# Kernel tuning notes

Hardware: AMD Instinct MI355X
Metric: run time of the kernel (lower is better)

Reference implementation:

```python
import jax, jax.numpy as jnp
import numpy as np

EPS = 1e-8
LN_EPS = 1e-6
B, S_IN, F, D, NH, MLP, L, O = 32, 512, 16, 512, 8, 2048, 4, 8
HD = D // NH

def softplus(x):
    return jnp.log1p(jnp.exp(x))

def apply_rope(x):
    # x: [B, S, D]; RoPE over full d_model, as in the original
    S, d = x.shape[1], x.shape[2]
    x1, x2 = x[..., ::2], x[..., 1::2]
    theta = jnp.arange(S)[:, None] / 10000 ** (jnp.arange(0, d, 2) / d)
    c, s = jnp.cos(theta)[None], jnp.sin(theta)[None]
    x1r = x1 * c - x2 * s
    x2r = x1 * s + x2 * c
    return jnp.stack([x1r, x2r], axis=-1).reshape(x.shape)

def layer_norm(x, g, b):
    mu = jnp.mean(x, axis=-1, keepdims=True)
    var = jnp.mean(jnp.square(x - mu), axis=-1, keepdims=True)
    return (x - mu) * jax.lax.rsqrt(var + LN_EPS) * g + b

def setup_inputs() -> dict:
    key = jax.random.key(0)
    ks = jax.random.split(key, 32)
    n = jax.random.normal
    d = {
        "x": n(ks[0], (B, S_IN, F), jnp.float32),
        "W_in": n(ks[1], (F, D)) * (1.0 / np.sqrt(F)),
        "b_in": jnp.zeros((D,)),
        "cls_tokens": n(ks[2], (1, O, D)) * 0.02,
        "Wqkv": n(ks[3], (L, D, 3 * D)) * (1.0 / np.sqrt(D)),
        "bqkv": jnp.zeros((L, 3 * D)),
        "Wo": n(ks[4], (L, D, D)) * (1.0 / np.sqrt(D)),
        "bo": jnp.zeros((L, D)),
        "ln1_g": jnp.ones((L, D)), "ln1_b": jnp.zeros((L, D)),
        "Wm1": n(ks[5], (L, D, MLP)) * (1.0 / np.sqrt(D)),
        "bm1": jnp.zeros((L, MLP)),
        "Wm2": n(ks[6], (L, MLP, D)) * (1.0 / np.sqrt(MLP)),
        "bm2": jnp.zeros((L, D)),
        "ln2_g": jnp.ones((L, D)), "ln2_b": jnp.zeros((L, D)),
        "Wh": n(ks[7], (O, D, D)) * (1.0 / np.sqrt(D)),
        "bh": jnp.zeros((O, D)),
        "mu_wmu": n(ks[8], (O, D)) * (1.0 / np.sqrt(D)),
        "mu_wrho": n(ks[9], (O, D)) * 0.001,
        "mu_bmu": jnp.zeros((O,)),
        "mu_brho": n(ks[10], (O,)) * 0.001,
        "lv_wmu": n(ks[11], (O, D)) * (1.0 / np.sqrt(D)),
        "lv_wrho": n(ks[12], (O, D)) * 0.001,
        "lv_bmu": jnp.zeros((O,)),
        "lv_brho": n(ks[13], (O,)) * 0.001,
        "eps_mu_w": n(ks[14], (O, D)),
        "eps_mu_b": n(ks[15], (O,)),
        "eps_lv_w": n(ks[16], (O, D)),
        "eps_lv_b": n(ks[17], (O,)),
    }
    return d

def reference(x, W_in, b_in, cls_tokens, Wqkv, bqkv, Wo, bo, ln1_g, ln1_b,
              Wm1, bm1, Wm2, bm2, ln2_g, ln2_b, Wh, bh,
              mu_wmu, mu_wrho, mu_bmu, mu_brho,
              lv_wmu, lv_wrho, lv_bmu, lv_brho,
              eps_mu_w, eps_mu_b, eps_lv_w, eps_lv_b):
    h = x @ W_in + b_in                                     # [B, S_IN, D]
    cls = jnp.tile(cls_tokens, (h.shape[0], 1, 1))
    h = jnp.concatenate([cls, h], axis=1)                   # [B, S, D]
    Bt, S, d = h.shape
    for l in range(L):
        qkv = h @ Wqkv[l] + bqkv[l]
        q, k, v = jnp.split(qkv, 3, axis=-1)
        q, k = apply_rope(q), apply_rope(k)
        q = q.reshape(Bt, S, NH, HD).transpose(0, 2, 1, 3)
        k = k.reshape(Bt, S, NH, HD).transpose(0, 2, 1, 3)
        v = v.reshape(Bt, S, NH, HD).transpose(0, 2, 1, 3)
        scores = jnp.einsum('bhid,bhjd->bhij', q, k) / jnp.sqrt(jnp.float32(HD))
        attn = jax.nn.softmax(scores, axis=-1)              # dropout off (eval)
        out = jnp.einsum('bhij,bhjd->bhid', attn, v)
        out = out.transpose(0, 2, 1, 3).reshape(Bt, S, d)
        out = out @ Wo[l] + bo[l]
        h = layer_norm(h + out, ln1_g[l], ln1_b[l])
        m = jax.nn.relu(h @ Wm1[l] + bm1[l]) @ Wm2[l] + bm2[l]
        h = layer_norm(h + m, ln2_g[l], ln2_b[l])
    x_cls = h[:, :O, :]                                     # [B, O, D]
    hid = jax.nn.relu(jnp.einsum('bod,odh->boh', x_cls, Wh) + bh[None])
    def var_head(wmu, wrho, bmu, brho, ew, eb):
        w = wmu + (softplus(wrho) + EPS) * ew               # [O, D]
        b = bmu + (softplus(brho) + EPS) * eb               # [O]
        return jnp.einsum('boh,oh->bo', hid, w) + b[None]
    mu = var_head(mu_wmu, mu_wrho, mu_bmu, mu_brho, eps_mu_w, eps_mu_b)
    lv = var_head(lv_wmu, lv_wrho, lv_bmu, lv_brho, eps_lv_w, eps_lv_b)
    lv = jnp.log(EPS + softplus(lv))
    return (mu, lv)
```

## Files before the change

### kernel.cpp

```cpp
#include <hip/hip_runtime.h>
#include <cstdint>


#define BATCH   32
#define SEQ     520
#define SP      576
#define DIM     512
#define NHEAD   8
#define HDIM    64
#define MLPD    2048
#define NLAYER  4
#define NROW    (BATCH * SEQ)
#define NPAIR   256

typedef __attribute__((ext_vector_type(4))) float  f32x4;
typedef __attribute__((ext_vector_type(8))) short  short8;

__device__ __forceinline__ unsigned short f2bf(float f) {
    unsigned u = __float_as_uint(f);
    unsigned r = (u + 0x7fffu + ((u >> 16) & 1u)) >> 16;
    return (unsigned short)r;
}
__device__ __forceinline__ float bf2f(short s) {
    return __uint_as_float(((unsigned)(unsigned short)s) << 16);
}
__device__ __forceinline__ unsigned cvt_pk_bf16(float lo, float hi) {
    unsigned r;
    asm("v_cvt_pk_bf16_f32 %0, %1, %2" : "=v"(r) : "v"(lo), "v"(hi));
    return r;
}
__device__ __forceinline__ float exp2_hw(float x) {
    float r;
    asm("v_exp_f32 %0, %1" : "=v"(r) : "v"(x));
    return r;
}
__device__ __forceinline__ float wred_sum(float v) {
    #pragma unroll
    for (int off = 32; off; off >>= 1) v += __shfl_xor(v, off);
    return v;
}

__device__ __forceinline__ void gload16(const void* g, void* l) {
    __builtin_amdgcn_global_load_lds(
        (const __attribute__((address_space(1))) unsigned int*)g,
        (__attribute__((address_space(3))) unsigned int*)l,
        16, 0, 0);
}

__global__ __launch_bounds__(256) void k_wconv(const float* __restrict__ src,
                                               short* __restrict__ dst,
                                               int K, int N) {
    src += (size_t)blockIdx.z * K * N;
    dst += (size_t)blockIdx.z * K * N;
    int n0 = blockIdx.x * 64, k0 = blockIdx.y * 64;
    __shared__ float t[64][65];
    int tid = threadIdx.x;
    int r = tid >> 2, cq = (tid & 3) * 16;
    const float* sp = src + (size_t)(k0 + r) * N + n0 + cq;
    #pragma unroll
    for (int e = 0; e < 16; e += 4) {
        float4 v = *(const float4*)(sp + e);
        t[r][cq + e] = v.x; t[r][cq + e + 1] = v.y;
        t[r][cq + e + 2] = v.z; t[r][cq + e + 3] = v.w;
    }
    __syncthreads();
    int n = tid >> 2, kq = (tid & 3) * 16;
    short* dp = dst + (size_t)(n0 + n) * K + k0 + kq;
    unsigned o0[4], o1[4];
    #pragma unroll
    for (int e = 0; e < 4; e++)
        o0[e] = cvt_pk_bf16(t[kq + 2 * e][n], t[kq + 2 * e + 1][n]);
    #pragma unroll
    for (int e = 0; e < 4; e++)
        o1[e] = cvt_pk_bf16(t[kq + 8 + 2 * e][n], t[kq + 9 + 2 * e][n]);
    *(uint4*)dp = make_uint4(o0[0], o0[1], o0[2], o0[3]);
    *(uint4*)(dp + 8) = make_uint4(o1[0], o1[1], o1[2], o1[3]);
}

__global__ void k_rope_tab(float2* __restrict__ tab) {
    int s = blockIdx.x, i = threadIdx.x;
    float fr = powf(10000.f, -2.f * (float)i / 512.f);
    float th = (float)s * fr;
    float sn, cn;
    sincosf(th, &sn, &cn);
    tab[s * NPAIR + i] = make_float2(cn, sn);
}

__global__ __launch_bounds__(256) void k_in_proj(const float* __restrict__ x,
                                                 const float* __restrict__ Wi,
                                                 const float* __restrict__ bi,
                                                 const float* __restrict__ cls,
                                                 short* __restrict__ hb) {
    int row = blockIdx.x;
    int b = row / SEQ, s = row % SEQ;
    bool is_cls = s < 8;
    float xr[16];
    if (!is_cls) {
        const float* xp = x + (size_t)(b * 512 + (s - 8)) * 16;
        #pragma unroll
        for (int f = 0; f < 16; f++) xr[f] = xp[f];
    }
    for (int c = threadIdx.x; c < DIM; c += 256) {
        float v;
        if (is_cls) {
            v = cls[s * DIM + c];
        } else {
            v = bi[c];
            #pragma unroll
            for (int f = 0; f < 16; f++) v = fmaf(xr[f], Wi[f * DIM + c], v);
        }
        hb[(size_t)row * DIM + c] = (short)f2bf(v);
    }
}

template <int BK, bool RELU, bool ADDRES>
__global__ __launch_bounds__(512) void k_gemm(const short* __restrict__ A,
                                              const short* __restrict__ Bt,
                                              const float* __restrict__ bias,
                                              const short* __restrict__ Res,
                                              short* __restrict__ Cout,
                                              int N, int K) {
    constexpr int NB  = BK / 8;
    constexpr int MSK = NB - 1;
    constexpr int SH  = (BK == 32) ? 1 : 0;
    constexpr int RPW = 64 / NB;
    constexpr int GPM = 128 / (8 * RPW);
    constexpr int NLD = 2 * GPM;
    __shared__ __align__(16) short As[2][128 * BK];
    __shared__ __align__(16) short Bs[2][128 * BK];
    const int tid = threadIdx.x;
    const int w = tid >> 6, l = tid & 63;

    const int chunk = gridDim.x >> 3;
    const int t = (blockIdx.x & 7) * chunk + (blockIdx.x >> 3);
    const int C = N >> 7;
    const int brow = (t / C) * 128, bcol = (t % C) * 128;

    const int srow = l / NB;
    const int sblk = l & MSK;
    const int soff = ((sblk ^ ((srow >> SH) & MSK)) * 8);
    const int fr = l & 15, t4 = l >> 4;
    const int wr = (w >> 2) * 64;
    const int wc = (w & 3) * 32;

    const short* Ab = A  + (size_t)(brow + w * RPW + srow) * K + soff;
    const short* Bb = Bt + (size_t)(bcol + w * RPW + srow) * K + soff;

    f32x4 acc[4][2];
    #pragma unroll
    for (int m = 0; m < 4; m++)
        #pragma unroll
        for (int n = 0; n < 2; n++) acc[m][n] = (f32x4){0.f, 0.f, 0.f, 0.f};

    auto stage = [&](int ko, int pb) {
        #pragma unroll
        for (int i = 0; i < GPM; i++)
            gload16(Ab + (size_t)(i * 8 * RPW) * K + ko,
                    &As[pb][(i * 8 * RPW + w * RPW) * BK]);
        #pragma unroll
        for (int i = 0; i < GPM; i++)
            gload16(Bb + (size_t)(i * 8 * RPW) * K + ko,
                    &Bs[pb][(i * 8 * RPW + w * RPW) * BK]);
    };

    const int nk = K / BK;
    stage(0, 0);
    stage(BK, 1);

    for (int kt = 0; kt < nk; ++kt) {
        const int cur = kt & 1;
        if (kt + 1 < nk) {
            if constexpr (NLD == 4) asm volatile("s_waitcnt vmcnt(4)" ::: "memory");
            else                    asm volatile("s_waitcnt vmcnt(2)" ::: "memory");
        } else {
            asm volatile("s_waitcnt vmcnt(0)" ::: "memory");
        }
        __builtin_amdgcn_s_barrier();
        __builtin_amdgcn_sched_barrier(0);

        short8 af[4][BK / 32], bf[2][BK / 32];
        #pragma unroll
        for (int m = 0; m < 4; m++) {
            int r = wr + m * 16 + fr;
            #pragma unroll
            for (int kk = 0; kk < BK / 32; kk++)
                af[m][kk] = *(const short8*)
                    &As[cur][r * BK + (((kk * 4 + t4) ^ ((r >> SH) & MSK)) * 8)];
        }
        #pragma unroll
        for (int n = 0; n < 2; n++) {
            int r = wc + n * 16 + fr;
            #pragma unroll
            for (int kk = 0; kk < BK / 32; kk++)
                bf[n][kk] = *(const short8*)
                    &Bs[cur][r * BK + (((kk * 4 + t4) ^ ((r >> SH) & MSK)) * 8)];
        }
        asm volatile("s_waitcnt lgkmcnt(0)" ::: "memory");
        __builtin_amdgcn_s_barrier();
        __builtin_amdgcn_sched_barrier(0);
        if (kt + 2 < nk) stage((kt + 2) * BK, cur);

        __builtin_amdgcn_s_setprio(1);
        #pragma unroll
        for (int kk = 0; kk < BK / 32; kk++)
            #pragma unroll
            for (int m = 0; m < 4; m++)
                #pragma unroll
                for (int n = 0; n < 2; n++)
                    acc[m][n] = __builtin_amdgcn_mfma_f32_16x16x32_bf16(
                        af[m][kk], bf[n][kk], acc[m][n], 0, 0, 0);
        __builtin_amdgcn_s_setprio(0);
    }

    const int r0 = (l >> 4) * 4, c0 = l & 15;
    #pragma unroll
    for (int m = 0; m < 4; m++) {
        #pragma unroll
        for (int n = 0; n < 2; n++) {
            int col = bcol + wc + n * 16 + c0;
            float bv = bias[col];
            #pragma unroll
            for (int q = 0; q < 4; q++) {
                int row = brow + wr + m * 16 + r0 + q;
                float v = acc[m][n][q] + bv;
                if (ADDRES) v += bf2f(Res[(size_t)row * N + col]);
                if (RELU) v = fmaxf(v, 0.f);
                Cout[(size_t)row * N + col] = (short)f2bf(v);
            }
        }
    }
}

template <int BK, bool RELU, bool ADDRES>
__global__ __launch_bounds__(256) void k_gemm64(const short* __restrict__ A,
                                                const short* __restrict__ Bt,
                                                const float* __restrict__ bias,
                                                const short* __restrict__ Res,
                                                short* __restrict__ Cout,
                                                int N, int K) {
    constexpr int NB  = BK / 8;
    constexpr int MSK = NB - 1;
    constexpr int SH  = (BK == 32) ? 1 : 0;
    constexpr int RPL = 512 / BK;
    constexpr int ALW = 128 / (4 * RPL);
    constexpr int BLW = 64 / (4 * RPL);
    constexpr int NLD = ALW + BLW;
    __shared__ __align__(16) short As[2][128 * BK];
    __shared__ __align__(16) short Bs[2][64 * BK];
    const int tid = threadIdx.x;
    const int w = tid >> 6, l = tid & 63;

    const int chunk = gridDim.x >> 3;
    const int t = (blockIdx.x & 7) * chunk + (blockIdx.x >> 3);
    const int C = N >> 6;
    const int brow = (t / C) * 128, bcol = (t % C) * 64;

    const int srow = l / NB;
    const int sblk = l & MSK;
    const int soff = ((sblk ^ ((srow >> SH) & MSK)) * 8);
    const int fr = l & 15, t4 = l >> 4;
    const int wr = (w >> 1) * 64;
    const int wc = (w & 1) * 32;

    f32x4 acc[4][2];
    #pragma unroll
    for (int m = 0; m < 4; m++)
        #pragma unroll
        for (int n = 0; n < 2; n++) acc[m][n] = (f32x4){0.f, 0.f, 0.f, 0.f};

    auto stage = [&](int ko, int pb) {
        #pragma unroll
        for (int i = 0; i < ALW; i++)
            gload16(A + (size_t)(brow + (w * ALW + i) * RPL + srow) * K + ko + soff,
                    &As[pb][((w * ALW + i) * RPL) * BK]);
        #pragma unroll
        for (int i = 0; i < BLW; i++)
            gload16(Bt + (size_t)(bcol + (w * BLW + i) * RPL + srow) * K + ko + soff,
                    &Bs[pb][((w * BLW + i) * RPL) * BK]);
    };

    const int nk = K / BK;
    stage(0, 0);
    stage(BK, 1);

    for (int kt = 0; kt < nk; ++kt) {
        const int cur = kt & 1;
        if (kt + 1 < nk) {
            if constexpr (NLD == 3) asm volatile("s_waitcnt vmcnt(3)" ::: "memory");
            else                    asm volatile("s_waitcnt vmcnt(6)" ::: "memory");
        } else {
            asm volatile("s_waitcnt vmcnt(0)" ::: "memory");
        }
        __builtin_amdgcn_s_barrier();
        __builtin_amdgcn_sched_barrier(0);

        short8 af[4][BK / 32], bf[2][BK / 32];
        #pragma unroll
        for (int m = 0; m < 4; m++) {
            int r = wr + m * 16 + fr;
            #pragma unroll
            for (int kk = 0; kk < BK / 32; kk++)
                af[m][kk] = *(const short8*)
                    &As[cur][r * BK + (((kk * 4 + t4) ^ ((r >> SH) & MSK)) * 8)];
        }
        #pragma unroll
        for (int n = 0; n < 2; n++) {
            int r = wc + n * 16 + fr;
            #pragma unroll
            for (int kk = 0; kk < BK / 32; kk++)
                bf[n][kk] = *(const short8*)
                    &Bs[cur][r * BK + (((kk * 4 + t4) ^ ((r >> SH) & MSK)) * 8)];
        }
        asm volatile("s_waitcnt lgkmcnt(0)" ::: "memory");
        __builtin_amdgcn_s_barrier();
        __builtin_amdgcn_sched_barrier(0);
        if (kt + 2 < nk) stage((kt + 2) * BK, cur);

        __builtin_amdgcn_s_setprio(1);
        #pragma unroll
        for (int kk = 0; kk < BK / 32; kk++)
            #pragma unroll
            for (int m = 0; m < 4; m++)
                #pragma unroll
                for (int n = 0; n < 2; n++)
                    acc[m][n] = __builtin_amdgcn_mfma_f32_16x16x32_bf16(
                        af[m][kk], bf[n][kk], acc[m][n], 0, 0, 0);
        __builtin_amdgcn_s_setprio(0);
    }

    const int r0 = (l >> 4) * 4, c0 = l & 15;
    #pragma unroll
    for (int m = 0; m < 4; m++) {
        #pragma unroll
        for (int n = 0; n < 2; n++) {
            int col = bcol + wc + n * 16 + c0;
            float bv = bias[col];
            #pragma unroll
            for (int q = 0; q < 4; q++) {
                int row = brow + wr + m * 16 + r0 + q;
                float v = acc[m][n][q] + bv;
                if (ADDRES) v += bf2f(Res[(size_t)row * N + col]);
                if (RELU) v = fmaxf(v, 0.f);
                Cout[(size_t)row * N + col] = (short)f2bf(v);
            }
        }
    }
}

__global__ __launch_bounds__(256) void k_kvprep(const short* __restrict__ qkv,
                                                const float2* __restrict__ tab,
                                                short* __restrict__ kbuf,
                                                short* __restrict__ vtbuf) {
    int bx = blockIdx.x;
    int jt = bx % 9, bh = bx / 9, b = bh >> 3, h = bh & 7;
    int tid = threadIdx.x;
    int row = tid >> 2, ch = tid & 3;
    int s = jt * 64 + row;
    bool valid = s < SEQ;
    size_t g = (size_t)(b * SEQ + (valid ? s : 0)) * 1536;

    short8 ok0 = (short8)0, ok1 = (short8)0;
    if (valid) {
        short8 k0 = *(const short8*)(qkv + g + 512 + h * 64 + ch * 16);
        short8 k1 = *(const short8*)(qkv + g + 512 + h * 64 + ch * 16 + 8);
        unsigned* u0 = (unsigned*)&ok0;
        unsigned* u1 = (unsigned*)&ok1;
        #pragma unroll
        for (int pp = 0; pp < 4; pp++) {
            float2 cs = tab[s * NPAIR + h * 32 + ch * 8 + pp];
            float x1 = bf2f(k0[2 * pp]), x2 = bf2f(k0[2 * pp + 1]);
            u0[pp] = cvt_pk_bf16(x1 * cs.x - x2 * cs.y, x1 * cs.y + x2 * cs.x);
            cs = tab[s * NPAIR + h * 32 + ch * 8 + 4 + pp];
            x1 = bf2f(k1[2 * pp]); x2 = bf2f(k1[2 * pp + 1]);
            u1[pp] = cvt_pk_bf16(x1 * cs.x - x2 * cs.y, x1 * cs.y + x2 * cs.x);
        }
    }
    short* kd = kbuf + ((size_t)bh * SP + jt * 64 + row) * 64 + ch * 16;
    *(short8*)kd = ok0;
    *(short8*)(kd + 8) = ok1;

    __shared__ short vt[64][72];
    short8 v0 = (short8)0, v1 = (short8)0;
    if (valid) {
        v0 = *(const short8*)(qkv + g + 1024 + h * 64 + ch * 16);
        v1 = *(const short8*)(qkv + g + 1024 + h * 64 + ch * 16 + 8);
    }
    *(short8*)&vt[row][ch * 16] = v0;
    *(short8*)&vt[row][ch * 16 + 8] = v1;
    __syncthreads();
    int d = row;
    short8 w0, w1;
    #pragma unroll
    for (int e = 0; e < 8; e++) w0[e] = vt[ch * 16 + e][d];
    #pragma unroll
    for (int e = 0; e < 8; e++) w1[e] = vt[ch * 16 + 8 + e][d];
    short* vd = vtbuf + ((size_t)bh * 64 + d) * SP + jt * 64 + ch * 16;
    *(short8*)vd = w0;
    *(short8*)(vd + 8) = w1;
}

__global__ __launch_bounds__(512) void k_attn_mfma(const short* __restrict__ qkv,
                                                   const short* __restrict__ kbuf,
                                                   const short* __restrict__ vtbuf,
                                                   const float2* __restrict__ tab,
                                                   short* __restrict__ aob) {
    __shared__ __align__(16) short Kl[2][64 * 64];
    __shared__ __align__(16) short Vl[2][64 * 64];
    __shared__ __align__(16) short sP[8][16][72];
    const int tid = threadIdx.x;
    const int w = tid >> 6, l = tid & 63;
    const int c = l & 15, t4 = l >> 4;
    int bx = blockIdx.x;
    int qt = bx >> 8, bh = bx & 255, b = bh >> 3, h = bh & 7;

    const float QSC = 0.125f * 1.44269504f;
    int q0 = qt * 128 + w * 16;
    int qrow = q0 + c;
    int qr = qrow < SEQ ? qrow : SEQ - 1;
    size_t gq = (size_t)(b * SEQ + qr) * 1536 + h * 64;
    short8 qf0 = *(const short8*)(qkv + gq + t4 * 8);
    short8 qf1 = *(const short8*)(qkv + gq + 32 + t4 * 8);
    {
        const float2* tq = tab + (size_t)qr * NPAIR + h * 32;
        unsigned* u0 = (unsigned*)&qf0;
        unsigned* u1 = (unsigned*)&qf1;
        #pragma unroll
        for (int pp = 0; pp < 4; pp++) {
            float2 cs = tq[t4 * 4 + pp];
            float x1 = bf2f(qf0[2 * pp]), x2 = bf2f(qf0[2 * pp + 1]);
            u0[pp] = cvt_pk_bf16((x1 * cs.x - x2 * cs.y) * QSC,
                                 (x1 * cs.y + x2 * cs.x) * QSC);
            cs = tq[16 + t4 * 4 + pp];
            x1 = bf2f(qf1[2 * pp]); x2 = bf2f(qf1[2 * pp + 1]);
            u1[pp] = cvt_pk_bf16((x1 * cs.x - x2 * cs.y) * QSC,
                                 (x1 * cs.y + x2 * cs.x) * QSC);
        }
    }

    f32x4 o0 = {0,0,0,0}, o1 = {0,0,0,0}, o2 = {0,0,0,0}, o3 = {0,0,0,0};
    float mrow[4] = {-1e30f, -1e30f, -1e30f, -1e30f};
    float lrow[4] = {0.f, 0.f, 0.f, 0.f};

    const short* kb = kbuf + (size_t)bh * SP * 64;
    const short* vb = vtbuf + (size_t)bh * 64 * SP;
    const int r1 = w * 8 + (l >> 3);
    const int blk = l & 7;

    auto stage = [&](int jt, int pb) {
        gload16(kb + ((size_t)(jt * 64 + r1)) * 64 + ((blk ^ (r1 & 7)) * 8),
                &Kl[pb][(w * 8) * 64]);
        gload16(vb + (size_t)r1 * SP + jt * 64 + ((blk ^ (r1 & 7)) * 8),
                &Vl[pb][(w * 8) * 64]);
    };

    stage(0, 0);
    stage(1, 1);

    for (int jt = 0; jt < 9; jt++) {
        const int cur = jt & 1;
        if (jt + 1 < 9) asm volatile("s_waitcnt vmcnt(2)" ::: "memory");
        else            asm volatile("s_waitcnt vmcnt(0)" ::: "memory");
        __builtin_amdgcn_s_barrier();
        __builtin_amdgcn_sched_barrier(0);

        f32x4 s0 = {0,0,0,0}, s1 = {0,0,0,0}, s2 = {0,0,0,0}, s3 = {0,0,0,0};
        __builtin_amdgcn_s_setprio(1);
        {
            int kr0 = c, kr1 = 16 + c, kr2 = 32 + c, kr3 = 48 + c;
            short8 kf;
            kf = *(const short8*)&Kl[cur][kr0 * 64 + ((t4 ^ (kr0 & 7)) * 8)];
            s0 = __builtin_amdgcn_mfma_f32_16x16x32_bf16(qf0, kf, s0, 0, 0, 0);
            kf = *(const short8*)&Kl[cur][kr0 * 64 + (((4 + t4) ^ (kr0 & 7)) * 8)];
            s0 = __builtin_amdgcn_mfma_f32_16x16x32_bf16(qf1, kf, s0, 0, 0, 0);
            kf = *(const short8*)&Kl[cur][kr1 * 64 + ((t4 ^ (kr1 & 7)) * 8)];
            s1 = __builtin_amdgcn_mfma_f32_16x16x32_bf16(qf0, kf, s1, 0, 0, 0);
            kf = *(const short8*)&Kl[cur][kr1 * 64 + (((4 + t4) ^ (kr1 & 7)) * 8)];
            s1 = __builtin_amdgcn_mfma_f32_16x16x32_bf16(qf1, kf, s1, 0, 0, 0);
            kf = *(const short8*)&Kl[cur][kr2 * 64 + ((t4 ^ (kr2 & 7)) * 8)];
            s2 = __builtin_amdgcn_mfma_f32_16x16x32_bf16(qf0, kf, s2, 0, 0, 0);
            kf = *(const short8*)&Kl[cur][kr2 * 64 + (((4 + t4) ^ (kr2 & 7)) * 8)];
            s2 = __builtin_amdgcn_mfma_f32_16x16x32_bf16(qf1, kf, s2, 0, 0, 0);
            kf = *(const short8*)&Kl[cur][kr3 * 64 + ((t4 ^ (kr3 & 7)) * 8)];
            s3 = __builtin_amdgcn_mfma_f32_16x16x32_bf16(qf0, kf, s3, 0, 0, 0);
            kf = *(const short8*)&Kl[cur][kr3 * 64 + (((4 + t4) ^ (kr3 & 7)) * 8)];
            s3 = __builtin_amdgcn_mfma_f32_16x16x32_bf16(qf1, kf, s3, 0, 0, 0);
        }
        __builtin_amdgcn_s_setprio(0);

        if (jt == 8) {
            #pragma unroll
            for (int r = 0; r < 4; r++) {
                if (c >= 8) s0[r] = -1e30f;
                s1[r] = -1e30f; s2[r] = -1e30f; s3[r] = -1e30f;
            }
        }

        #pragma unroll
        for (int r = 0; r < 4; r++) {
            float pmax = fmaxf(fmaxf(s0[r], s1[r]), fmaxf(s2[r], s3[r]));
            if (!__all(pmax <= mrow[r] + 8.f)) {
                float mx = pmax;
                mx = fmaxf(mx, __shfl_xor(mx, 1));
                mx = fmaxf(mx, __shfl_xor(mx, 2));
                mx = fmaxf(mx, __shfl_xor(mx, 4));
                mx = fmaxf(mx, __shfl_xor(mx, 8));
                if (mx > mrow[r]) {
                    float sc = exp2_hw(mrow[r] - mx);
                    mrow[r] = mx;
                    lrow[r] *= sc;
                    o0[r] *= sc; o1[r] *= sc; o2[r] *= sc; o3[r] *= sc;
                }
            }
            float p0 = exp2_hw(s0[r] - mrow[r]);
            float p1 = exp2_hw(s1[r] - mrow[r]);
            float p2 = exp2_hw(s2[r] - mrow[r]);
            float p3 = exp2_hw(s3[r] - mrow[r]);
            lrow[r] += (p0 + p1) + (p2 + p3);
            unsigned pk01 = cvt_pk_bf16(p0, p1);
            unsigned pk23 = cvt_pk_bf16(p2, p3);
            int q = t4 * 4 + r;
            sP[w][q][c]      = (short)(pk01 & 0xffff);
            sP[w][q][16 + c] = (short)(pk01 >> 16);
            sP[w][q][32 + c] = (short)(pk23 & 0xffff);
            sP[w][q][48 + c] = (short)(pk23 >> 16);
        }

        __builtin_amdgcn_s_setprio(1);
        {
            short8 pf0 = *(const short8*)&sP[w][c][t4 * 8];
            short8 pf1 = *(const short8*)&sP[w][c][32 + t4 * 8];
            int vr0 = c, vr1 = 16 + c, vr2 = 32 + c, vr3 = 48 + c;
            short8 vf;
            vf = *(const short8*)&Vl[cur][vr0 * 64 + ((t4 ^ (vr0 & 7)) * 8)];
            o0 = __builtin_amdgcn_mfma_f32_16x16x32_bf16(pf0, vf, o0, 0, 0, 0);
            vf = *(const short8*)&Vl[cur][vr0 * 64 + (((4 + t4) ^ (vr0 & 7)) * 8)];
            o0 = __builtin_amdgcn_mfma_f32_16x16x32_bf16(pf1, vf, o0, 0, 0, 0);
            vf = *(const short8*)&Vl[cur][vr1 * 64 + ((t4 ^ (vr1 & 7)) * 8)];
            o1 = __builtin_amdgcn_mfma_f32_16x16x32_bf16(pf0, vf, o1, 0, 0, 0);
            vf = *(const short8*)&Vl[cur][vr1 * 64 + (((4 + t4) ^ (vr1 & 7)) * 8)];
            o1 = __builtin_amdgcn_mfma_f32_16x16x32_bf16(pf1, vf, o1, 0, 0, 0);
            vf = *(const short8*)&Vl[cur][vr2 * 64 + ((t4 ^ (vr2 & 7)) * 8)];
            o2 = __builtin_amdgcn_mfma_f32_16x16x32_bf16(pf0, vf, o2, 0, 0, 0);
            vf = *(const short8*)&Vl[cur][vr2 * 64 + (((4 + t4) ^ (vr2 & 7)) * 8)];
            o2 = __builtin_amdgcn_mfma_f32_16x16x32_bf16(pf1, vf, o2, 0, 0, 0);
            vf = *(const short8*)&Vl[cur][vr3 * 64 + ((t4 ^ (vr3 & 7)) * 8)];
            o3 = __builtin_amdgcn_mfma_f32_16x16x32_bf16(pf0, vf, o3, 0, 0, 0);
            vf = *(const short8*)&Vl[cur][vr3 * 64 + (((4 + t4) ^ (vr3 & 7)) * 8)];
            o3 = __builtin_amdgcn_mfma_f32_16x16x32_bf16(pf1, vf, o3, 0, 0, 0);
        }
        __builtin_amdgcn_s_setprio(0);

        asm volatile("s_waitcnt lgkmcnt(0)" ::: "memory");
        __builtin_amdgcn_s_barrier();
        __builtin_amdgcn_sched_barrier(0);
        if (jt + 2 < 9) stage(jt + 2, cur);
    }

    #pragma unroll
    for (int r = 0; r < 4; r++) {
        float s = lrow[r];
        s += __shfl_xor(s, 1);
        s += __shfl_xor(s, 2);
        s += __shfl_xor(s, 4);
        s += __shfl_xor(s, 8);
        int q = q0 + t4 * 4 + r;
        if (q < SEQ) {
            float inv = 1.f / s;
            short* ao = aob + ((size_t)(b * SEQ + q)) * DIM + h * 64 + c;
            ao[0]  = (short)f2bf(o0[r] * inv);
            ao[16] = (short)f2bf(o1[r] * inv);
            ao[32] = (short)f2bf(o2[r] * inv);
            ao[48] = (short)f2bf(o3[r] * inv);
        }
    }
}

__global__ __launch_bounds__(256) void k_ln(short* __restrict__ hb,
                                            const short* __restrict__ sum,
                                            const float* __restrict__ g,
                                            const float* __restrict__ bta) {
    int row = blockIdx.x * 4 + (threadIdx.x >> 6);
    int l = threadIdx.x & 63;
    size_t base = (size_t)row * DIM + l * 8;
    short8 hv = *(const short8*)&sum[base];
    float a[8];
    float s1 = 0.f, s2 = 0.f;
    #pragma unroll
    for (int e = 0; e < 8; e++) {
        a[e] = bf2f(hv[e]);
        s1 += a[e];
        s2 += a[e] * a[e];
    }
    s1 = wred_sum(s1);
    s2 = wred_sum(s2);
    float mu = s1 * (1.f / 512.f);
    float rr = rsqrtf(s2 * (1.f / 512.f) - mu * mu + 1e-6f);
    float4 g0 = *(const float4*)&g[l * 8];
    float4 g1 = *(const float4*)&g[l * 8 + 4];
    float4 b0 = *(const float4*)&bta[l * 8];
    float4 b1 = *(const float4*)&bta[l * 8 + 4];
    unsigned o[4];
    o[0] = cvt_pk_bf16((a[0] - mu) * rr * g0.x + b0.x,
                       (a[1] - mu) * rr * g0.y + b0.y);
    o[1] = cvt_pk_bf16((a[2] - mu) * rr * g0.z + b0.z,
                       (a[3] - mu) * rr * g0.w + b0.w);
    o[2] = cvt_pk_bf16((a[4] - mu) * rr * g1.x + b1.x,
                       (a[5] - mu) * rr * g1.y + b1.y);
    o[3] = cvt_pk_bf16((a[6] - mu) * rr * g1.z + b1.z,
                       (a[7] - mu) * rr * g1.w + b1.w);
    *(uint4*)&hb[base] = make_uint4(o[0], o[1], o[2], o[3]);
}

__global__ __launch_bounds__(256) void k_hid(const short* __restrict__ hb,
                                             const float* __restrict__ Wh,
                                             const float* __restrict__ bh,
                                             float* __restrict__ hid) {
    int j = blockIdx.x * 256 + threadIdx.x;
    int o = blockIdx.y, b = blockIdx.z;
    const short* xr = hb + ((size_t)(b * SEQ + o)) * DIM;
    const float* wcol = Wh + (size_t)o * DIM * DIM + j;
    float acc = bh[o * DIM + j];
    #pragma unroll 8
    for (int d = 0; d < DIM; d++)
        acc = fmaf(bf2f(xr[d]), wcol[(size_t)d * DIM], acc);
    hid[((size_t)b * 8 + o) * DIM + j] = fmaxf(acc, 0.f);
}

__device__ __forceinline__ float softplus_f(float x) { return log1pf(expf(x)); }

__global__ __launch_bounds__(64) void k_var(const float* __restrict__ hid,
                                            const float* __restrict__ mu_wmu,
                                            const float* __restrict__ mu_wrho,
                                            const float* __restrict__ mu_bmu,
                                            const float* __restrict__ mu_brho,
                                            const float* __restrict__ lv_wmu,
                                            const float* __restrict__ lv_wrho,
                                            const float* __restrict__ lv_bmu,
                                            const float* __restrict__ lv_brho,
                                            const float* __restrict__ eps_mu_w,
                                            const float* __restrict__ eps_mu_b,
                                            const float* __restrict__ eps_lv_w,
                                            const float* __restrict__ eps_lv_b,
                                            float* __restrict__ out) {
    const float EPS = 1e-8f;
    int bo = blockIdx.x;
    int o = bo & 7;
    int l = threadIdx.x;
    float am = 0.f, al = 0.f;
    #pragma unroll
    for (int k = 0; k < 8; k++) {
        int d = k * 64 + l;
        int od = o * DIM + d;
        float hv = hid[(size_t)bo * DIM + d];
        am = fmaf(hv, mu_wmu[od] + (softplus_f(mu_wrho[od]) + EPS) * eps_mu_w[od], am);
        al = fmaf(hv, lv_wmu[od] + (softplus_f(lv_wrho[od]) + EPS) * eps_lv_w[od], al);
    }
    am = wred_sum(am);
    al = wred_sum(al);
    if (l == 0) {
        float mu = am + mu_bmu[o] + (softplus_f(mu_brho[o]) + EPS) * eps_mu_b[o];
        out[bo] = mu;
        float lvv = al + lv_bmu[o] + (softplus_f(lv_brho[o]) + EPS) * eps_lv_b[o];
        out[256 + bo] = logf(EPS + softplus_f(lvv));
    }
}

extern "C" void kernel_launch(void* const* d_in, const int* in_sizes, int n_in,
                              void* d_out, int out_size, void* d_ws, size_t ws_size,
                              hipStream_t stream) {
    const float* x      = (const float*)d_in[0];
    const float* W_in   = (const float*)d_in[1];
    const float* b_in   = (const float*)d_in[2];
    const float* cls    = (const float*)d_in[3];
    const float* Wqkv   = (const float*)d_in[4];
    const float* bqkv   = (const float*)d_in[5];
    const float* Wo     = (const float*)d_in[6];
    const float* bo     = (const float*)d_in[7];
    const float* ln1_g  = (const float*)d_in[8];
    const float* ln1_b  = (const float*)d_in[9];
    const float* Wm1    = (const float*)d_in[10];
    const float* bm1    = (const float*)d_in[11];
    const float* Wm2    = (const float*)d_in[12];
    const float* bm2    = (const float*)d_in[13];
    const float* ln2_g  = (const float*)d_in[14];
    const float* ln2_b  = (const float*)d_in[15];
    const float* Wh     = (const float*)d_in[16];
    const float* bh     = (const float*)d_in[17];
    const float* mu_wmu = (const float*)d_in[18];
    const float* mu_wrho= (const float*)d_in[19];
    const float* mu_bmu = (const float*)d_in[20];
    const float* mu_brho= (const float*)d_in[21];
    const float* lv_wmu = (const float*)d_in[22];
    const float* lv_wrho= (const float*)d_in[23];
    const float* lv_bmu = (const float*)d_in[24];
    const float* lv_brho= (const float*)d_in[25];
    const float* e_mu_w = (const float*)d_in[26];
    const float* e_mu_b = (const float*)d_in[27];
    const float* e_lv_w = (const float*)d_in[28];
    const float* e_lv_b = (const float*)d_in[29];
    float* out = (float*)d_out;

    char* p = (char*)d_ws;
    auto alloc = [&](size_t bytes) {
        char* r = p;
        p += (bytes + 255) & ~(size_t)255;
        return r;
    };
    const size_t qkv_bytes = (size_t)NROW * 1536 * 2;
    const size_t kbuf_bytes = (size_t)BATCH * NHEAD * SP * 64 * 2;
    const size_t attn_bytes = qkv_bytes + 2 * kbuf_bytes + 512;
    const size_t mid_bytes = (size_t)NROW * MLPD * 2;
    char*   U1    =          alloc(attn_bytes > mid_bytes ? attn_bytes : mid_bytes);
    short*  qkv   = (short*)U1;
    short*  kbuf  = (short*)(U1 + ((qkv_bytes + 255) & ~(size_t)255));
    short*  vtbuf = kbuf + kbuf_bytes / 2;
    short*  mid   = (short*)U1;
    short*  hb    = (short*) alloc((size_t)NROW * DIM * 2);
    short*  deltab= (short*) alloc((size_t)NROW * DIM * 2);
    short*  aob   = (short*) alloc((size_t)NROW * DIM * 2);
    short*  wqkvt = (short*) alloc((size_t)NLAYER * 1536 * 512 * 2);
    short*  wot   = (short*) alloc((size_t)NLAYER * 512 * 512 * 2);
    short*  wm1t  = (short*) alloc((size_t)NLAYER * 2048 * 512 * 2);
    short*  wm2t  = (short*) alloc((size_t)NLAYER * 512 * 2048 * 2);
    float2* ropet = (float2*)alloc((size_t)SEQ * NPAIR * 8);
    float*  hid   = (float*) alloc((size_t)256 * DIM * 4);

    k_wconv<<<dim3(24, 8, 4), 256, 0, stream>>>(Wqkv, wqkvt, 512, 1536);
    k_wconv<<<dim3(8, 8, 4),  256, 0, stream>>>(Wo,   wot,   512, 512);
    k_wconv<<<dim3(32, 8, 4), 256, 0, stream>>>(Wm1,  wm1t,  512, 2048);
    k_wconv<<<dim3(8, 32, 4), 256, 0, stream>>>(Wm2,  wm2t,  2048, 512);
    k_rope_tab<<<SEQ, NPAIR, 0, stream>>>(ropet);
    k_in_proj<<<NROW, 256, 0, stream>>>(x, W_in, b_in, cls, hb);

    const int RT = NROW / 128;
    for (int l = 0; l < NLAYER; l++) {
        k_gemm<32, false, false><<<RT * 12, 512, 0, stream>>>(
            hb, wqkvt + (size_t)l * 1536 * 512, bqkv + l * 1536, nullptr, qkv, 1536, 512);
        k_kvprep<<<BATCH * NHEAD * 9, 256, 0, stream>>>(qkv, ropet, kbuf, vtbuf);
        k_attn_mfma<<<5 * 256, 512, 0, stream>>>(qkv, kbuf, vtbuf, ropet, aob);
        k_gemm64<32, false, true><<<RT * 8, 256, 0, stream>>>(
            aob, wot + (size_t)l * 512 * 512, bo + l * 512, hb, deltab, 512, 512);
        k_ln<<<NROW / 4, 256, 0, stream>>>(hb, deltab, ln1_g + l * 512, ln1_b + l * 512);
        k_gemm<32, true, false><<<RT * 16, 512, 0, stream>>>(
            hb, wm1t + (size_t)l * 2048 * 512, bm1 + l * 2048, nullptr, mid, 2048, 512);
        k_gemm64<64, false, true><<<RT * 8, 256, 0, stream>>>(
            mid, wm2t + (size_t)l * 512 * 2048, bm2 + l * 512, hb, deltab, 512, 2048);
        k_ln<<<NROW / 4, 256, 0, stream>>>(hb, deltab, ln2_g + l * 512, ln2_b + l * 512);
    }

    k_hid<<<dim3(2, 8, 32), 256, 0, stream>>>(hb, Wh, bh, hid);
    k_var<<<256, 64, 0, stream>>>(hid, mu_wmu, mu_wrho, mu_bmu, mu_brho,
                                  lv_wmu, lv_wrho, lv_bmu, lv_brho,
                                  e_mu_w, e_mu_b, e_lv_w, e_lv_b, out);
}
```

Measured before the change: 1.023 ms.

## Fuse RoPE, Q scaling and K/V layout scatter into QKV GEMM epilogue

The QKV projection GEMM epilogue now applies RoPE to Q and K, using a lane shuffle to fetch each element's pair partner. It pre-scales Q, and writes Q, K and transposed V directly into the per-head buffers that attention consumes. This removes the separate kvprep kernel and the Q RoPE step inside the attention kernel, saving a full read and write of the QKV tensor and one launch per layer. In exchange, the epilogue does scattered 2-byte stores, and the transposed V writes are poorly coalesced. The padded sequence rows of the K/V buffers are no longer zeroed, so they keep leftover data from the aliased MLP buffer.

```diff
diff --git a/kernel.cpp b/kernel.cpp
--- a/kernel.cpp
+++ b/kernel.cpp
@@ -113,12 +113,14 @@
     }
 }
 
-template <int BK, bool RELU, bool ADDRES>
+template <int BK, bool RELU, bool QKVOUT>
 __global__ __launch_bounds__(512) void k_gemm(const short* __restrict__ A,
                                               const short* __restrict__ Bt,
                                               const float* __restrict__ bias,
-                                              const short* __restrict__ Res,
                                               short* __restrict__ Cout,
+                                              short* __restrict__ kb2,
+                                              short* __restrict__ vt2,
+                                              const float2* __restrict__ tab,
                                               int N, int K) {
     constexpr int NB  = BK / 8;
     constexpr int MSK = NB - 1;
@@ -213,6 +215,7 @@
     }
 
     const int r0 = (l >> 4) * 4, c0 = l & 15;
+    const float QSC = 0.125f * 1.44269504f;
     #pragma unroll
     for (int m = 0; m < 4; m++) {
         #pragma unroll
@@ -223,15 +226,36 @@
             for (int q = 0; q < 4; q++) {
                 int row = brow + wr + m * 16 + r0 + q;
                 float v = acc[m][n][q] + bv;
-                if (ADDRES) v += bf2f(Res[(size_t)row * N + col]);
-                if (RELU) v = fmaxf(v, 0.f);
-                Cout[(size_t)row * N + col] = (short)f2bf(v);
+                if (QKVOUT) {
+                    int bb = row / SEQ, s = row - bb * SEQ;
+                    if (col < 1024) {
+                        float vo = __shfl_xor(v, 1);
+                        int i = (col & 511) >> 1;
+                        float2 cs = tab[s * NPAIR + i];
+                        float o = (c0 & 1) ? (vo * cs.y + v * cs.x)
+                                           : (v * cs.x - vo * cs.y);
+                        if (col < 512) {
+                            Cout[(size_t)row * 512 + col] = (short)f2bf(o * QSC);
+                        } else {
+                            int ck = col - 512, h = ck >> 6, d = ck & 63;
+                            kb2[(((size_t)(bb * 8 + h)) * SP + s) * 64 + d] =
+                                (short)f2bf(o);
+                        }
+                    } else {
+                        int cv = col - 1024, h = cv >> 6, d = cv & 63;
+                        vt2[(((size_t)(bb * 8 + h)) * 64 + d) * SP + s] =
+                            (short)f2bf(v);
+                    }
+                } else {
+                    if (RELU) v = fmaxf(v, 0.f);
+                    Cout[(size_t)row * N + col] = (short)f2bf(v);
+                }
             }
         }
     }
 }
 
-template <int BK, bool RELU, bool ADDRES>
+template <int BK, bool ADDRES>
 __global__ __launch_bounds__(256) void k_gemm64(const short* __restrict__ A,
                                                 const short* __restrict__ Bt,
                                                 const float* __restrict__ bias,
@@ -340,69 +364,15 @@
                 int row = brow + wr + m * 16 + r0 + q;
                 float v = acc[m][n][q] + bv;
                 if (ADDRES) v += bf2f(Res[(size_t)row * N + col]);
-                if (RELU) v = fmaxf(v, 0.f);
                 Cout[(size_t)row * N + col] = (short)f2bf(v);
             }
         }
     }
 }
 
-__global__ __launch_bounds__(256) void k_kvprep(const short* __restrict__ qkv,
-                                                const float2* __restrict__ tab,
-                                                short* __restrict__ kbuf,
-                                                short* __restrict__ vtbuf) {
-    int bx = blockIdx.x;
-    int jt = bx % 9, bh = bx / 9, b = bh >> 3, h = bh & 7;
-    int tid = threadIdx.x;
-    int row = tid >> 2, ch = tid & 3;
-    int s = jt * 64 + row;
-    bool valid = s < SEQ;
-    size_t g = (size_t)(b * SEQ + (valid ? s : 0)) * 1536;
-
-    short8 ok0 = (short8)0, ok1 = (short8)0;
-    if (valid) {
-        short8 k0 = *(const short8*)(qkv + g + 512 + h * 64 + ch * 16);
-        short8 k1 = *(const short8*)(qkv + g + 512 + h * 64 + ch * 16 + 8);
-        unsigned* u0 = (unsigned*)&ok0;
-        unsigned* u1 = (unsigned*)&ok1;
-        #pragma unroll
-        for (int pp = 0; pp < 4; pp++) {
-            float2 cs = tab[s * NPAIR + h * 32 + ch * 8 + pp];
-            float x1 = bf2f(k0[2 * pp]), x2 = bf2f(k0[2 * pp + 1]);
-            u0[pp] = cvt_pk_bf16(x1 * cs.x - x2 * cs.y, x1 * cs.y + x2 * cs.x);
-            cs = tab[s * NPAIR + h * 32 + ch * 8 + 4 + pp];
-            x1 = bf2f(k1[2 * pp]); x2 = bf2f(k1[2 * pp + 1]);
-            u1[pp] = cvt_pk_bf16(x1 * cs.x - x2 * cs.y, x1 * cs.y + x2 * cs.x);
-        }
-    }
-    short* kd = kbuf + ((size_t)bh * SP + jt * 64 + row) * 64 + ch * 16;
-    *(short8*)kd = ok0;
-    *(short8*)(kd + 8) = ok1;
-
-    __shared__ short vt[64][72];
-    short8 v0 = (short8)0, v1 = (short8)0;
-    if (valid) {
-        v0 = *(const short8*)(qkv + g + 1024 + h * 64 + ch * 16);
-        v1 = *(const short8*)(qkv + g + 1024 + h * 64 + ch * 16 + 8);
-    }
-    *(short8*)&vt[row][ch * 16] = v0;
-    *(short8*)&vt[row][ch * 16 + 8] = v1;
-    __syncthreads();
-    int d = row;
-    short8 w0, w1;
-    #pragma unroll
-    for (int e = 0; e < 8; e++) w0[e] = vt[ch * 16 + e][d];
-    #pragma unroll
-    for (int e = 0; e < 8; e++) w1[e] = vt[ch * 16 + 8 + e][d];
-    short* vd = vtbuf + ((size_t)bh * 64 + d) * SP + jt * 64 + ch * 16;
-    *(short8*)vd = w0;
-    *(short8*)(vd + 8) = w1;
-}
-
-__global__ __launch_bounds__(512) void k_attn_mfma(const short* __restrict__ qkv,
+__global__ __launch_bounds__(512) void k_attn_mfma(const short* __restrict__ qbuf,
                                                    const short* __restrict__ kbuf,
                                                    const short* __restrict__ vtbuf,
-                                                   const float2* __restrict__ tab,
                                                    short* __restrict__ aob) {
     __shared__ __align__(16) short Kl[2][64 * 64];
     __shared__ __align__(16) short Vl[2][64 * 64];
@@ -413,29 +383,12 @@
     int bx = blockIdx.x;
     int qt = bx >> 8, bh = bx & 255, b = bh >> 3, h = bh & 7;
 
-    const float QSC = 0.125f * 1.44269504f;
     int q0 = qt * 128 + w * 16;
     int qrow = q0 + c;
     int qr = qrow < SEQ ? qrow : SEQ - 1;
-    size_t gq = (size_t)(b * SEQ + qr) * 1536 + h * 64;
-    short8 qf0 = *(const short8*)(qkv + gq + t4 * 8);
-    short8 qf1 = *(const short8*)(qkv + gq + 32 + t4 * 8);
-    {
-        const float2* tq = tab + (size_t)qr * NPAIR + h * 32;
-        unsigned* u0 = (unsigned*)&qf0;
-        unsigned* u1 = (unsigned*)&qf1;
-        #pragma unroll
-        for (int pp = 0; pp < 4; pp++) {
-            float2 cs = tq[t4 * 4 + pp];
-            float x1 = bf2f(qf0[2 * pp]), x2 = bf2f(qf0[2 * pp + 1]);
-            u0[pp] = cvt_pk_bf16((x1 * cs.x - x2 * cs.y) * QSC,
-                                 (x1 * cs.y + x2 * cs.x) * QSC);
-            cs = tq[16 + t4 * 4 + pp];
-            x1 = bf2f(qf1[2 * pp]); x2 = bf2f(qf1[2 * pp + 1]);
-            u1[pp] = cvt_pk_bf16((x1 * cs.x - x2 * cs.y) * QSC,
-                                 (x1 * cs.y + x2 * cs.x) * QSC);
-        }
-    }
+    size_t gq = (size_t)(b * SEQ + qr) * 512 + h * 64;
+    short8 qf0 = *(const short8*)(qbuf + gq + t4 * 8);
+    short8 qf1 = *(const short8*)(qbuf + gq + 32 + t4 * 8);
 
     f32x4 o0 = {0,0,0,0}, o1 = {0,0,0,0}, o2 = {0,0,0,0}, o3 = {0,0,0,0};
     float mrow[4] = {-1e30f, -1e30f, -1e30f, -1e30f};
@@ -706,13 +659,13 @@
         p += (bytes + 255) & ~(size_t)255;
         return r;
     };
-    const size_t qkv_bytes = (size_t)NROW * 1536 * 2;
+    const size_t qbuf_bytes = (size_t)NROW * 512 * 2;
     const size_t kbuf_bytes = (size_t)BATCH * NHEAD * SP * 64 * 2;
-    const size_t attn_bytes = qkv_bytes + 2 * kbuf_bytes + 512;
-    const size_t mid_bytes = (size_t)NROW * MLPD * 2;
+    const size_t attn_bytes = qbuf_bytes + 2 * kbuf_bytes + 1024;
+    const size_t mid_bytes  = (size_t)NROW * MLPD * 2;
     char*   U1    =          alloc(attn_bytes > mid_bytes ? attn_bytes : mid_bytes);
-    short*  qkv   = (short*)U1;
-    short*  kbuf  = (short*)(U1 + ((qkv_bytes + 255) & ~(size_t)255));
+    short*  qbuf  = (short*)U1;
+    short*  kbuf  = (short*)(U1 + ((qbuf_bytes + 255) & ~(size_t)255));
     short*  vtbuf = kbuf + kbuf_bytes / 2;
     short*  mid   = (short*)U1;
     short*  hb    = (short*) alloc((size_t)NROW * DIM * 2);
@@ -734,16 +687,17 @@
 
     const int RT = NROW / 128;
     for (int l = 0; l < NLAYER; l++) {
-        k_gemm<32, false, false><<<RT * 12, 512, 0, stream>>>(
-            hb, wqkvt + (size_t)l * 1536 * 512, bqkv + l * 1536, nullptr, qkv, 1536, 512);
-        k_kvprep<<<BATCH * NHEAD * 9, 256, 0, stream>>>(qkv, ropet, kbuf, vtbuf);
-        k_attn_mfma<<<5 * 256, 512, 0, stream>>>(qkv, kbuf, vtbuf, ropet, aob);
-        k_gemm64<32, false, true><<<RT * 8, 256, 0, stream>>>(
+        k_gemm<32, false, true><<<RT * 12, 512, 0, stream>>>(
+            hb, wqkvt + (size_t)l * 1536 * 512, bqkv + l * 1536,
+            qbuf, kbuf, vtbuf, ropet, 1536, 512);
+        k_attn_mfma<<<5 * 256, 512, 0, stream>>>(qbuf, kbuf, vtbuf, aob);
+        k_gemm64<32, true><<<RT * 8, 256, 0, stream>>>(
             aob, wot + (size_t)l * 512 * 512, bo + l * 512, hb, deltab, 512, 512);
         k_ln<<<NROW / 4, 256, 0, stream>>>(hb, deltab, ln1_g + l * 512, ln1_b + l * 512);
         k_gemm<32, true, false><<<RT * 16, 512, 0, stream>>>(
-            hb, wm1t + (size_t)l * 2048 * 512, bm1 + l * 2048, nullptr, mid, 2048, 512);
-        k_gemm64<64, false, true><<<RT * 8, 256, 0, stream>>>(
+            hb, wm1t + (size_t)l * 2048 * 512, bm1 + l * 2048,
+            mid, nullptr, nullptr, nullptr, 2048, 512);
+        k_gemm64<64, true><<<RT * 8, 256, 0, stream>>>(
             mid, wm2t + (size_t)l * 512 * 2048, bm2 + l * 512, hb, deltab, 512, 2048);
         k_ln<<<NROW / 4, 256, 0, stream>>>(hb, deltab, ln2_g + l * 512, ln2_b + l * 512);
     }
```

After: 1.102 ms. 1.08x slower.
